# Optimization experiments

Measured on AMD Instinct MI355X. Metric: run time of the kernel, lower is better.

Reference implementation:

```python
import jax, jax.numpy as jnp
import numpy as np


def setup_inputs() -> dict:
    key = jax.random.key(0)
    ks = jax.random.split(key, 6)
    B, S, D_IN, D_OUT, E, R = 4, 2048, 4096, 4096, 8, 16
    x = jax.random.normal(ks[0], (B, S, D_IN), dtype=jnp.float32)
    probs = jax.random.uniform(ks[1], (B, E), dtype=jnp.float32)
    router_probs = probs / jnp.sum(probs, axis=-1, keepdims=True)
    weight = jax.random.normal(ks[2], (D_OUT, D_IN), dtype=jnp.float32) * 0.02
    bias = jax.random.normal(ks[3], (D_OUT,), dtype=jnp.float32) * 0.02
    lora_A = jax.random.normal(ks[4], (E, R, D_IN), dtype=jnp.float32) * 0.02
    lora_B = jax.random.normal(ks[5], (E, D_OUT, R), dtype=jnp.float32) * 0.02
    return {"x": x, "router_probs": router_probs, "weight": weight,
            "bias": bias, "lora_A": lora_A, "lora_B": lora_B}


def reference(x, router_probs, weight, bias, lora_A, lora_B):
    scaling = 2.0
    # base linear: [b,s,i] @ [o,i]^T + bias
    base_out = jnp.einsum('bsi,oi->bso', x, weight) + bias
    # low-rank per-expert projection: [b,s,e,r] (small: r=16)
    mid = jnp.einsum('bsi,eri->bser', x, lora_A)
    # weight by router probs (per batch, per expert) before up-projection
    mid_w = mid * router_probs[:, None, :, None]
    # sum over experts fused into the up-projection contraction
    delta = jnp.einsum('bser,eor->bso', mid_w, lora_B) * scaling
    return base_out + delta
```

## Files before the change

kernel.cpp:

```cpp
#include <hip/hip_runtime.h>


typedef _Float16 half8 __attribute__((ext_vector_type(8)));
typedef _Float16 half4 __attribute__((ext_vector_type(4)));
typedef float    f32x4 __attribute__((ext_vector_type(4)));

#define M_TOT 8192
#define N_TOT 4096
#define K_IN  4096
#define KA    4224
#define NT    66

__device__ __forceinline__ void cvt_store4(_Float16* p, float4 f) {
  half4 h;
  h[0] = (_Float16)f.x; h[1] = (_Float16)f.y;
  h[2] = (_Float16)f.z; h[3] = (_Float16)f.w;
  *(half4*)p = h;
}

template <int LOG2C, int DCOLS>
__global__ __launch_bounds__(256) void convert_f32_f16_t(
    const float* __restrict__ src, _Float16* __restrict__ dst, int total8) {
  for (int i = blockIdx.x * 256 + threadIdx.x; i < total8;
       i += gridDim.x * 256) {
    int base = i << 3;
    int r = base >> LOG2C;
    int c = base & ((1 << LOG2C) - 1);
    const float4* s = (const float4*)(src + (size_t)base);
    float4 f0 = s[0], f1 = s[1];
    half8 h;
    h[0]=(_Float16)f0.x; h[1]=(_Float16)f0.y; h[2]=(_Float16)f0.z; h[3]=(_Float16)f0.w;
    h[4]=(_Float16)f1.x; h[5]=(_Float16)f1.y; h[6]=(_Float16)f1.z; h[7]=(_Float16)f1.w;
    *(half8*)(dst + (size_t)r * DCOLS + c) = h;
  }
}

__global__ __launch_bounds__(256) void wtail_gather_f16(
    const float* __restrict__ loraB, _Float16* __restrict__ Wa) {
  int idx = blockIdx.x * 256 + threadIdx.x;
  int n = idx >> 7, j = idx & 127;
  int e = j >> 4, r = j & 15;
  Wa[(size_t)n * KA + K_IN + j] =
      (_Float16)loraB[((size_t)e * N_TOT + n) * 16 + r];
}

__global__ __launch_bounds__(256) void lorabf_gather_f32(
    const float* __restrict__ loraB, float* __restrict__ lorabf) {
  int idx = blockIdx.x * 256 + threadIdx.x;
  int n = idx >> 7, j = idx & 127;
  int e = j >> 4, r = j & 15;
  lorabf[(size_t)n * 128 + j] = loraB[((size_t)e * N_TOT + n) * 16 + r];
}

__global__ __launch_bounds__(256) void mid2_kernel(
    _Float16* __restrict__ Xa, const _Float16* __restrict__ lAh,
    const float* __restrict__ router) {
  __shared__ _Float16 As[32 * 64];
  __shared__ _Float16 Bs[128 * 64];
  int tid = threadIdx.x, lane = tid & 63, w = tid >> 6;
  int m0 = blockIdx.x * 32;
  int b = m0 >> 11;
  f32x4 acc[2][2] = {};

  for (int ks = 0; ks < 64; ++ks) {
    int kb = ks * 128;
    {
      const char* s = (const char*)Xa +
          (size_t)(m0 + w * 8 + (lane >> 3)) * (KA * 2) + kb + (lane & 7) * 16;
      __builtin_amdgcn_global_load_lds(
          (const __attribute__((address_space(1))) void*)s,
          (__attribute__((address_space(3))) void*)((char*)As + w * 1024), 16, 0, 0);
    }
#pragma unroll
    for (int i = 0; i < 4; ++i) {
      const char* s = (const char*)lAh +
          (size_t)((w * 4 + i) * 8 + (lane >> 3)) * (4096 * 2) + kb + (lane & 7) * 16;
      __builtin_amdgcn_global_load_lds(
          (const __attribute__((address_space(1))) void*)s,
          (__attribute__((address_space(3))) void*)((char*)Bs + (w * 4 + i) * 1024), 16, 0, 0);
    }
    __syncthreads();
#pragma unroll
    for (int kk = 0; kk < 2; ++kk) {
      half8 a[2], bf[2];
#pragma unroll
      for (int mi = 0; mi < 2; ++mi)
        a[mi] = *(const half8*)(As + (mi * 16 + (lane & 15)) * 64 + kk * 32 + (lane >> 4) * 8);
#pragma unroll
      for (int ni = 0; ni < 2; ++ni)
        bf[ni] = *(const half8*)(Bs + (w * 32 + ni * 16 + (lane & 15)) * 64 + kk * 32 + (lane >> 4) * 8);
#pragma unroll
      for (int mi = 0; mi < 2; ++mi)
#pragma unroll
        for (int ni = 0; ni < 2; ++ni)
          acc[mi][ni] = __builtin_amdgcn_mfma_f32_16x16x32_f16(a[mi], bf[ni], acc[mi][ni], 0, 0, 0);
    }
    __syncthreads();
  }

#pragma unroll
  for (int ni = 0; ni < 2; ++ni) {
    int j = w * 32 + ni * 16 + (lane & 15);
    int e = j >> 4;
    float sc = 2.0f * router[b * 8 + e];
#pragma unroll
    for (int mi = 0; mi < 2; ++mi) {
      f32x4 v = acc[mi][ni];
#pragma unroll
      for (int jj = 0; jj < 4; ++jj) {
        int m = m0 + mi * 16 + (lane >> 4) * 4 + jj;
        Xa[(size_t)m * KA + K_IN + j] = (_Float16)(v[jj] * sc);
      }
    }
  }
}

__global__ __launch_bounds__(256) void mid_kernel(
    const float* __restrict__ x, const float* __restrict__ loraA,
    const float* __restrict__ router, float* __restrict__ midw) {
  __shared__ _Float16 As[32 * 64];
  __shared__ _Float16 Bs[128 * 64];
  int tid = threadIdx.x, lane = tid & 63, w = tid >> 6;
  int m0 = blockIdx.x * 32;
  int b = m0 >> 11;
  f32x4 acc[2][2] = {};
  for (int ks = 0; ks < 64; ++ks) {
    int k0 = ks * 64;
#pragma unroll
    for (int it = 0; it < 2; ++it) {
      int idx = tid + it * 256;
      int r = idx >> 4, c4 = idx & 15;
      float4 f = *(const float4*)(x + (size_t)(m0 + r) * K_IN + k0 + c4 * 4);
      cvt_store4(As + r * 64 + c4 * 4, f);
    }
#pragma unroll
    for (int it = 0; it < 8; ++it) {
      int idx = tid + it * 256;
      int r = idx >> 4, c4 = idx & 15;
      float4 f = *(const float4*)(loraA + (size_t)r * K_IN + k0 + c4 * 4);
      cvt_store4(Bs + r * 64 + c4 * 4, f);
    }
    __syncthreads();
#pragma unroll
    for (int kk = 0; kk < 2; ++kk) {
      half8 a[2], bf[2];
#pragma unroll
      for (int mi = 0; mi < 2; ++mi)
        a[mi] = *(const half8*)(As + (mi * 16 + (lane & 15)) * 64 + kk * 32 + (lane >> 4) * 8);
#pragma unroll
      for (int ni = 0; ni < 2; ++ni)
        bf[ni] = *(const half8*)(Bs + (w * 32 + ni * 16 + (lane & 15)) * 64 + kk * 32 + (lane >> 4) * 8);
#pragma unroll
      for (int mi = 0; mi < 2; ++mi)
#pragma unroll
        for (int ni = 0; ni < 2; ++ni)
          acc[mi][ni] = __builtin_amdgcn_mfma_f32_16x16x32_f16(a[mi], bf[ni], acc[mi][ni], 0, 0, 0);
    }
    __syncthreads();
  }
#pragma unroll
  for (int ni = 0; ni < 2; ++ni) {
    int j = w * 32 + ni * 16 + (lane & 15);
    int e = j >> 4;
    float sc = 2.0f * router[b * 8 + e];
#pragma unroll
    for (int mi = 0; mi < 2; ++mi) {
      f32x4 v = acc[mi][ni];
#pragma unroll
      for (int jj = 0; jj < 4; ++jj) {
        int m = m0 + mi * 16 + (lane >> 4) * 4 + jj;
        midw[(size_t)m * 128 + j] = v[jj] * sc;
      }
    }
  }
}

#define BAR    __builtin_amdgcn_s_barrier()
#define SCHED0 __builtin_amdgcn_sched_barrier(0)
#define PRIO1  __builtin_amdgcn_s_setprio(1)
#define PRIO0  __builtin_amdgcn_s_setprio(0)
#define VMW0   asm volatile("s_waitcnt vmcnt(0)" ::: "memory")
#define GLOAD(src, dst) __builtin_amdgcn_global_load_lds( \
    (const __attribute__((address_space(1))) void*)(src), \
    (__attribute__((address_space(3))) void*)(dst), 16, 0, 0)

#define READ_A(aF, mb, buf) do { \
  _Pragma("unroll") for (int mi = 0; mi < 4; ++mi) { \
    int row = wm + ((mb) + mi) * 16 + ln15; \
    _Pragma("unroll") for (int kk = 0; kk < 2; ++kk) \
      aF[mi][kk] = *(const half8*)((const char*)(buf) + row * 128 + \
                                   (((kk * 4 + ln4) ^ ln7) * 16)); \
  } } while (0)

#define READ_B(bF, nb, buf) do { \
  _Pragma("unroll") for (int ni = 0; ni < 2; ++ni) { \
    int row = wn + ((nb) + ni) * 16 + ln15; \
    _Pragma("unroll") for (int kk = 0; kk < 2; ++kk) \
      bF[ni][kk] = *(const half8*)((const char*)(buf) + row * 128 + \
                                   (((kk * 4 + ln4) ^ ln7) * 16)); \
  } } while (0)

#define MFMA_Q(aF, bF, mb, nb) do { \
  PRIO1; \
  _Pragma("unroll") for (int kk = 0; kk < 2; ++kk) \
    _Pragma("unroll") for (int mi = 0; mi < 4; ++mi) \
      _Pragma("unroll") for (int ni = 0; ni < 2; ++ni) \
        acc[(mb) + mi][(nb) + ni] = __builtin_amdgcn_mfma_f32_16x16x32_f16( \
            aF[mi][kk], bF[ni][kk], acc[(mb) + mi][(nb) + ni], 0, 0, 0); \
  PRIO0; \
  } while (0)

#define STAGE(tt, bufA, bufB) do { \
  const char* sA_ = XpC + (size_t)(tt) * 128; \
  const char* sB_ = WpC + (size_t)(tt) * 128; \
  GLOAD(sA_ + off[0][0], (char*)(bufA) + lds_off[0][0]); \
  GLOAD(sA_ + off[0][1], (char*)(bufA) + lds_off[0][1]); \
  GLOAD(sA_ + off[1][0], (char*)(bufA) + lds_off[1][0]); \
  GLOAD(sA_ + off[1][1], (char*)(bufA) + lds_off[1][1]); \
  GLOAD(sB_ + off[0][0], (char*)(bufB) + lds_off[0][0]); \
  GLOAD(sB_ + off[0][1], (char*)(bufB) + lds_off[0][1]); \
  GLOAD(sB_ + off[1][0], (char*)(bufB) + lds_off[1][0]); \
  GLOAD(sB_ + off[1][1], (char*)(bufB) + lds_off[1][1]); \
  } while (0)

__global__ __launch_bounds__(512, 2) void gemm256(
    const _Float16* __restrict__ Xa, const _Float16* __restrict__ Wa,
    const float* __restrict__ bias, float* __restrict__ out) {
  __shared__ _Float16 As[2][256 * 64];
  __shared__ _Float16 Bs[2][256 * 64];

  int tid = threadIdx.x, lane = tid & 63, w = tid >> 6;
  int ln15 = lane & 15, ln4 = lane >> 4, ln7 = lane & 7;
  int wm = (w >> 2) * 128, wn = (w & 3) * 64;

  int bid = blockIdx.x;
  int xcd = bid & 7, idx = bid >> 3;
  int mt = (xcd & 3) * 8 + (idx & 7);
  int nt = (xcd >> 2) * 8 + (idx >> 3);
  int m0 = mt << 8, n0 = nt << 8;

  const char* XpC = (const char*)Xa + (size_t)m0 * (KA * 2);
  const char* WpC = (const char*)Wa + (size_t)n0 * (KA * 2);

  int lrow = lane >> 3;
  int scol = ((lane & 7) ^ lrow) * 16;
  int off[2][2], lds_off[2][2];
#pragma unroll
  for (int h = 0; h < 2; ++h)
#pragma unroll
    for (int j = 0; j < 2; ++j) {
      int rbase = h * 128 + w * 16 + j * 8;
      off[h][j] = (rbase + lrow) * (KA * 2) + scol;
      lds_off[h][j] = rbase * 128;
    }

  f32x4 acc[8][4] = {};

  STAGE(0, &As[0][0], &Bs[0][0]);
  VMW0; BAR; SCHED0;

#pragma unroll 1
  for (int t = 0; t < NT; ++t) {
    const _Float16* cA = As[t & 1];
    const _Float16* cB = Bs[t & 1];
    if (t < NT - 1) STAGE(t + 1, &As[(t + 1) & 1][0], &Bs[(t + 1) & 1][0]);

    half8 a0[4][2], a4[4][2], b01[2][2], b23[2][2];
    READ_A(a0, 0, cA);
    READ_B(b01, 0, cB);
    READ_B(b23, 2, cB);
    MFMA_Q(a0, b01, 0, 0);
    READ_A(a4, 4, cA);
    MFMA_Q(a0, b23, 0, 2);
    MFMA_Q(a4, b23, 4, 2);
    MFMA_Q(a4, b01, 4, 0);

    if (t < NT - 1) { VMW0; BAR; SCHED0; }
  }

#pragma unroll
  for (int ni = 0; ni < 4; ++ni) {
    int n = n0 + wn + ni * 16 + ln15;
    float bz = bias[n];
#pragma unroll
    for (int mi = 0; mi < 8; ++mi) {
      f32x4 v = acc[mi][ni];
      int mb = m0 + wm + mi * 16 + ln4 * 4;
#pragma unroll
      for (int jj = 0; jj < 4; ++jj)
        out[(size_t)(mb + jj) * N_TOT + n] = v[jj] + bz;
    }
  }
}

__global__ __launch_bounds__(256) void gemm_fallback(
    const float* __restrict__ x, const float* __restrict__ wgt,
    const float* __restrict__ midw, const float* __restrict__ lorabf,
    const float* __restrict__ bias, float* __restrict__ out) {
  __shared__ _Float16 As[128 * 64];
  __shared__ _Float16 Bs[128 * 64];
  int tid = threadIdx.x, lane = tid & 63, w = tid >> 6;
  int mt = blockIdx.x & 63, nt = blockIdx.x >> 6;
  int m0 = mt << 7, n0 = nt << 7;
  int wm = (w >> 1) * 64, wn = (w & 1) * 64;
  f32x4 acc[4][4] = {};
  for (int ks = 0; ks < NT; ++ks) {
    int k0 = ks * 64;
    const float *asrc, *bsrc; size_t astr, bstr; int ac, bc;
    if (ks < 64) { asrc = x;    astr = K_IN; ac = k0;        bsrc = wgt;    bstr = K_IN; bc = k0; }
    else         { asrc = midw; astr = 128;  ac = k0 - K_IN; bsrc = lorabf; bstr = 128;  bc = k0 - K_IN; }
#pragma unroll
    for (int it = 0; it < 8; ++it) {
      int idx = tid + it * 256;
      int r = idx >> 4, c4 = idx & 15;
      float4 fa = *(const float4*)(asrc + (size_t)(m0 + r) * astr + ac + c4 * 4);
      cvt_store4(As + r * 64 + c4 * 4, fa);
      float4 fb = *(const float4*)(bsrc + (size_t)(n0 + r) * bstr + bc + c4 * 4);
      cvt_store4(Bs + r * 64 + c4 * 4, fb);
    }
    __syncthreads();
#pragma unroll
    for (int kk = 0; kk < 2; ++kk) {
      half8 a[4], bf[4];
#pragma unroll
      for (int mi = 0; mi < 4; ++mi)
        a[mi] = *(const half8*)(As + (wm + mi * 16 + (lane & 15)) * 64 + kk * 32 + (lane >> 4) * 8);
#pragma unroll
      for (int ni = 0; ni < 4; ++ni)
        bf[ni] = *(const half8*)(Bs + (wn + ni * 16 + (lane & 15)) * 64 + kk * 32 + (lane >> 4) * 8);
#pragma unroll
      for (int mi = 0; mi < 4; ++mi)
#pragma unroll
        for (int ni = 0; ni < 4; ++ni)
          acc[mi][ni] = __builtin_amdgcn_mfma_f32_16x16x32_f16(a[mi], bf[ni], acc[mi][ni], 0, 0, 0);
    }
    __syncthreads();
  }
#pragma unroll
  for (int ni = 0; ni < 4; ++ni) {
    int n = n0 + wn + ni * 16 + (lane & 15);
    float bz = bias[n];
#pragma unroll
    for (int mi = 0; mi < 4; ++mi) {
      f32x4 v = acc[mi][ni];
      int mbase = m0 + wm + mi * 16 + (lane >> 4) * 4;
#pragma unroll
      for (int jj = 0; jj < 4; ++jj)
        out[(size_t)(mbase + jj) * N_TOT + n] = v[jj] + bz;
    }
  }
}

extern "C" void kernel_launch(void* const* d_in, const int* in_sizes, int n_in,
                              void* d_out, int out_size, void* d_ws, size_t ws_size,
                              hipStream_t stream) {
  const float* x      = (const float*)d_in[0];
  const float* router = (const float*)d_in[1];
  const float* wgt    = (const float*)d_in[2];
  const float* bias   = (const float*)d_in[3];
  const float* loraA  = (const float*)d_in[4];
  const float* loraB  = (const float*)d_in[5];
  float* out = (float*)d_out;
  char* ws = (char*)d_ws;

  const size_t XAUG_B = (size_t)M_TOT * KA * 2;
  const size_t WAUG_B = (size_t)N_TOT * KA * 2;
  const size_t LAH_B  = (size_t)128 * K_IN * 2;
  const size_t MIDW_B = (size_t)M_TOT * 128 * 4;
  bool fast = ws_size >= XAUG_B + WAUG_B + LAH_B;

  if (fast) {
    _Float16* Xa  = (_Float16*)ws;
    _Float16* Wa  = (_Float16*)(ws + XAUG_B);
    _Float16* lAh = (_Float16*)(ws + XAUG_B + WAUG_B);
    convert_f32_f16_t<12, KA><<<2048, 256, 0, stream>>>(x,   Xa, M_TOT * K_IN / 8);
    convert_f32_f16_t<12, KA><<<2048, 256, 0, stream>>>(wgt, Wa, N_TOT * K_IN / 8);
    convert_f32_f16_t<12, 4096><<<256, 256, 0, stream>>>(loraA, lAh, 128 * K_IN / 8);
    wtail_gather_f16<<<2048, 256, 0, stream>>>(loraB, Wa);
    mid2_kernel<<<256, 256, 0, stream>>>(Xa, lAh, router);
    gemm256<<<512, 512, 0, stream>>>(Xa, Wa, bias, out);
  } else {
    float* midw   = (float*)ws;
    float* lorabf = (float*)(ws + MIDW_B);
    lorabf_gather_f32<<<2048, 256, 0, stream>>>(loraB, lorabf);
    mid_kernel<<<256, 256, 0, stream>>>(x, loraA, router, midw);
    gemm_fallback<<<2048, 256, 0, stream>>>(x, wgt, midw, lorabf, bias, out);
  }
}
```

Before: 397.8 us.

## Split K-tile into half planes and interleave loads with MFMA phases

Each 64-wide K tile in LDS is split into two 32-wide planes with a new swizzle. The main loop becomes four phases in which LDS fragment reads, global-to-LDS prefetch issue and 16-MFMA bursts are interleaved, separated by barriers and partial vmcnt waits. The goal is to overlap memory traffic with MFMA work in a ping-pong style and to cut register pressure from fragment buffers. The cost is many more barriers per iteration, which may stall waves.

```diff
diff --git a/kernel.cpp b/kernel.cpp
--- a/kernel.cpp
+++ b/kernel.cpp
@@ -179,58 +179,49 @@
 #define SCHED0 __builtin_amdgcn_sched_barrier(0)
 #define PRIO1  __builtin_amdgcn_s_setprio(1)
 #define PRIO0  __builtin_amdgcn_s_setprio(0)
+#define LGKM0  do { asm volatile("s_waitcnt lgkmcnt(0)" ::: "memory"); \
+                    __builtin_amdgcn_sched_barrier(0); } while (0)
+#define VMW4   asm volatile("s_waitcnt vmcnt(4)" ::: "memory")
 #define VMW0   asm volatile("s_waitcnt vmcnt(0)" ::: "memory")
 #define GLOAD(src, dst) __builtin_amdgcn_global_load_lds( \
     (const __attribute__((address_space(1))) void*)(src), \
     (__attribute__((address_space(3))) void*)(dst), 16, 0, 0)
 
-#define READ_A(aF, mb, buf) do { \
-  _Pragma("unroll") for (int mi = 0; mi < 4; ++mi) { \
-    int row = wm + ((mb) + mi) * 16 + ln15; \
-    _Pragma("unroll") for (int kk = 0; kk < 2; ++kk) \
-      aF[mi][kk] = *(const half8*)((const char*)(buf) + row * 128 + \
-                                   (((kk * 4 + ln4) ^ ln7) * 16)); \
-  } } while (0)
-
-#define READ_B(bF, nb, buf) do { \
-  _Pragma("unroll") for (int ni = 0; ni < 2; ++ni) { \
-    int row = wn + ((nb) + ni) * 16 + ln15; \
-    _Pragma("unroll") for (int kk = 0; kk < 2; ++kk) \
-      bF[ni][kk] = *(const half8*)((const char*)(buf) + row * 128 + \
-                                   (((kk * 4 + ln4) ^ ln7) * 16)); \
-  } } while (0)
-
-#define MFMA_Q(aF, bF, mb, nb) do { \
+#define STAGEH(srcbase, t1, kh, plane) do { \
+  const char* s_ = (srcbase) + (size_t)(t1) * 128 + (kh) * 64; \
+  GLOAD(s_ + goff0, (char*)(plane) + loff0); \
+  GLOAD(s_ + goff1, (char*)(plane) + loff1); \
+  } while (0)
+
+#define READ_A4(aF, mb, plane) do { \
+  _Pragma("unroll") for (int mi = 0; mi < 4; ++mi) \
+    aF[mi] = *(const half8*)((const char*)(plane) + \
+                             (wm + ((mb) + mi) * 16 + ln15) * 64 + rslot); \
+  } while (0)
+
+#define READ_B4(bF, plane) do { \
+  _Pragma("unroll") for (int ni = 0; ni < 4; ++ni) \
+    bF[ni] = *(const half8*)((const char*)(plane) + \
+                             (wn + ni * 16 + ln15) * 64 + rslot); \
+  } while (0)
+
+#define MFMA_Q16(aF, bF, mb) do { \
   PRIO1; \
-  _Pragma("unroll") for (int kk = 0; kk < 2; ++kk) \
-    _Pragma("unroll") for (int mi = 0; mi < 4; ++mi) \
-      _Pragma("unroll") for (int ni = 0; ni < 2; ++ni) \
-        acc[(mb) + mi][(nb) + ni] = __builtin_amdgcn_mfma_f32_16x16x32_f16( \
-            aF[mi][kk], bF[ni][kk], acc[(mb) + mi][(nb) + ni], 0, 0, 0); \
+  _Pragma("unroll") for (int mi = 0; mi < 4; ++mi) \
+    _Pragma("unroll") for (int ni = 0; ni < 4; ++ni) \
+      acc[(mb) + mi][ni] = __builtin_amdgcn_mfma_f32_16x16x32_f16( \
+          aF[mi], bF[ni], acc[(mb) + mi][ni], 0, 0, 0); \
   PRIO0; \
-  } while (0)
-
-#define STAGE(tt, bufA, bufB) do { \
-  const char* sA_ = XpC + (size_t)(tt) * 128; \
-  const char* sB_ = WpC + (size_t)(tt) * 128; \
-  GLOAD(sA_ + off[0][0], (char*)(bufA) + lds_off[0][0]); \
-  GLOAD(sA_ + off[0][1], (char*)(bufA) + lds_off[0][1]); \
-  GLOAD(sA_ + off[1][0], (char*)(bufA) + lds_off[1][0]); \
-  GLOAD(sA_ + off[1][1], (char*)(bufA) + lds_off[1][1]); \
-  GLOAD(sB_ + off[0][0], (char*)(bufB) + lds_off[0][0]); \
-  GLOAD(sB_ + off[0][1], (char*)(bufB) + lds_off[0][1]); \
-  GLOAD(sB_ + off[1][0], (char*)(bufB) + lds_off[1][0]); \
-  GLOAD(sB_ + off[1][1], (char*)(bufB) + lds_off[1][1]); \
   } while (0)
 
 __global__ __launch_bounds__(512, 2) void gemm256(
     const _Float16* __restrict__ Xa, const _Float16* __restrict__ Wa,
     const float* __restrict__ bias, float* __restrict__ out) {
-  __shared__ _Float16 As[2][256 * 64];
-  __shared__ _Float16 Bs[2][256 * 64];
+  __shared__ _Float16 As[2][2][256 * 32];
+  __shared__ _Float16 Bs[2][2][256 * 32];
 
   int tid = threadIdx.x, lane = tid & 63, w = tid >> 6;
-  int ln15 = lane & 15, ln4 = lane >> 4, ln7 = lane & 7;
+  int ln15 = lane & 15, ln4 = lane >> 4;
   int wm = (w >> 2) * 128, wn = (w & 3) * 64;
 
   int bid = blockIdx.x;
@@ -242,40 +233,46 @@
   const char* XpC = (const char*)Xa + (size_t)m0 * (KA * 2);
   const char* WpC = (const char*)Wa + (size_t)n0 * (KA * 2);
 
-  int lrow = lane >> 3;
-  int scol = ((lane & 7) ^ lrow) * 16;
-  int off[2][2], lds_off[2][2];
-#pragma unroll
-  for (int h = 0; h < 2; ++h)
-#pragma unroll
-    for (int j = 0; j < 2; ++j) {
-      int rbase = h * 128 + w * 16 + j * 8;
-      off[h][j] = (rbase + lrow) * (KA * 2) + scol;
-      lds_off[h][j] = rbase * 128;
-    }
+  int sslot16 = (((lane & 3) ^ ((lane >> 3) & 3)) * 16);
+  int goff0 = ((2 * w + 0) * 16 + (lane >> 2)) * (KA * 2) + sslot16;
+  int goff1 = ((2 * w + 1) * 16 + (lane >> 2)) * (KA * 2) + sslot16;
+  int loff0 = (2 * w + 0) * 1024 + lane * 16;
+  int loff1 = (2 * w + 1) * 1024 + lane * 16;
+
+  int rslot = ((ln4 ^ ((lane >> 1) & 3)) * 16);
 
   f32x4 acc[8][4] = {};
-
-  STAGE(0, &As[0][0], &Bs[0][0]);
+  half8 aF[4], bF[4];
+
+  STAGEH(XpC, 0, 0, As[0][0]); STAGEH(WpC, 0, 0, Bs[0][0]);
+  STAGEH(XpC, 0, 1, As[0][1]); STAGEH(WpC, 0, 1, Bs[0][1]);
   VMW0; BAR; SCHED0;
 
 #pragma unroll 1
   for (int t = 0; t < NT; ++t) {
-    const _Float16* cA = As[t & 1];
-    const _Float16* cB = Bs[t & 1];
-    if (t < NT - 1) STAGE(t + 1, &As[(t + 1) & 1][0], &Bs[(t + 1) & 1][0]);
-
-    half8 a0[4][2], a4[4][2], b01[2][2], b23[2][2];
-    READ_A(a0, 0, cA);
-    READ_B(b01, 0, cB);
-    READ_B(b23, 2, cB);
-    MFMA_Q(a0, b01, 0, 0);
-    READ_A(a4, 4, cA);
-    MFMA_Q(a0, b23, 0, 2);
-    MFMA_Q(a4, b23, 4, 2);
-    MFMA_Q(a4, b01, 4, 0);
-
-    if (t < NT - 1) { VMW0; BAR; SCHED0; }
+    int cur = t & 1, nxt = cur ^ 1;
+    bool pf = (t < NT - 1);
+
+    READ_A4(aF, 0, As[cur][0]);
+    READ_B4(bF, Bs[cur][0]);
+    if (pf) STAGEH(XpC, t + 1, 0, As[nxt][0]);
+    BAR; LGKM0; MFMA_Q16(aF, bF, 0); BAR;
+
+    READ_A4(aF, 4, As[cur][0]);
+    if (pf) STAGEH(WpC, t + 1, 0, Bs[nxt][0]);
+    BAR; LGKM0; MFMA_Q16(aF, bF, 4);
+    if (pf) { VMW4; } else { VMW0; }
+    BAR; SCHED0;
+
+    READ_A4(aF, 0, As[cur][1]);
+    READ_B4(bF, Bs[cur][1]);
+    if (pf) STAGEH(XpC, t + 1, 1, As[nxt][1]);
+    BAR; LGKM0; MFMA_Q16(aF, bF, 0); BAR;
+
+    READ_A4(aF, 4, As[cur][1]);
+    if (pf) STAGEH(WpC, t + 1, 1, Bs[nxt][1]);
+    BAR; LGKM0; MFMA_Q16(aF, bF, 4);
+    if (pf) { VMW4; BAR; SCHED0; }
   }
 
 #pragma unroll
```

Result: slower. 406.0 us (+2.1%).
